# Performance work log

Measured on AMD Instinct MI355X. Metric: run time of the kernel, lower is better.

The kernel has to match this reference:

```python
import jax, jax.numpy as jnp
import numpy as np


def setup_inputs() -> dict:
    key = jax.random.key(0)
    k1, k2 = jax.random.split(key)
    inp = jax.random.normal(k1, (32, 1, 128, 128), dtype=jnp.float32)
    mask = (jax.random.uniform(k2, (32, 1, 1, 128)) < 0.25).astype(jnp.float32)
    return {"input": inp, "mask": mask}


def reference(input, mask):
    # Faithful to KSpaceMap.forward: `mask` is accepted but never used there.
    # Original: k = RFFT(x) (unnormalized full 2D FFT via torch.rfft onesided=False),
    # repeat W times, zero all but column i, then IFFT2 (torch.ifft, includes 1/(H*W)),
    # keep the real channel -> out[b, i, h, w].
    # Because the mask is a one-hot frequency column, ifft2 factorizes analytically:
    #   ifft2(onehot_col_i(k)) = (1/W) * ifft_h(k)[:, i] outer exp(2*pi*j*i*w/W)
    # which avoids materializing the [B, W, 2, H, W] repeated k-space.
    B, _, H, W = input.shape
    x = input[:, 0, :, :]                              # [B, H, W]
    k = jnp.fft.fft2(x)                                # [B, H, W] complex, unnormalized FFT
    A = jnp.fft.ifft(k, axis=-2)                       # ifft over height (1/H included): [B, H, W]
    w = jnp.arange(W)
    phase = 2.0 * jnp.pi * jnp.outer(w, w).astype(jnp.float32) / W   # [W(i), W(w)]
    Pr = jnp.cos(phase) / W                            # real part of DFT basis / W
    Pi = jnp.sin(phase) / W                            # imag part of DFT basis / W
    # out[b, i, h, w] = Re(A[b, h, i] * P[i, w])
    out = (jnp.einsum('bhi,iw->bihw', A.real.astype(jnp.float32), Pr)
           - jnp.einsum('bhi,iw->bihw', A.imag.astype(jnp.float32), Pi))
    return out
```

## Files before the change

### kernel.cpp

```cpp
#include <hip/hip_runtime.h>
#include <math.h>


typedef float f32x4 __attribute__((ext_vector_type(4)));

__device__ __forceinline__ void dft_plane(const float* xs, int i, int half,
                                          float& arO, float& aiO) {
    float sstep, cstep;
    sincospif((float)i * (1.0f / 64.0f), &sstep, &cstep);
    const float dc = cstep, ds = -sstep;
    float ar = 0.0f, ai = 0.0f;
#pragma unroll
    for (int ch = 0; ch < 2; ++ch) {
        const int u0 = half * 64 + ch * 32;
        const int a0 = (i * u0) & 127;
        float s0, c0;
        sincospif((float)a0 * (1.0f / 64.0f), &s0, &c0);
        float cr = c0, ci = -s0;
#pragma unroll
        for (int j2 = 0; j2 < 32; ++j2) {
            const float xv = xs[ch * 32 + j2];
            ar = fmaf(xv, cr, ar);
            ai = fmaf(xv, ci, ai);
            const float ncr = fmaf(cr, dc, -ci * ds);
            ci = fmaf(cr, ds, ci * dc);
            cr = ncr;
        }
    }
    ar += __shfl_xor(ar, 1);
    ai += __shfl_xor(ai, 1);
    arO = ar * (1.0f / 128.0f);
    aiO = ai * (1.0f / 128.0f);
}

__global__ __launch_bounds__(256) void kspace_v6(const float* __restrict__ x,
                                                 float* __restrict__ out) {
    const int blk  = blockIdx.x;
    const int b    = blk >> 5;
    const int g    = blk & 31;
    const int t    = threadIdx.x;
    const int wv   = t >> 6;
    const int lane = t & 63;
    const int h    = wv * 32 + (lane >> 1);
    const int half = lane & 1;

    const float* xp = x + ((size_t)b * 128 + h) * 128 + half * 64;
    float xs[64];
#pragma unroll
    for (int j = 0; j < 16; ++j) {
        const f32x4 v = ((const f32x4*)xp)[j];
        xs[4 * j + 0] = v.x;
        xs[4 * j + 1] = v.y;
        xs[4 * j + 2] = v.z;
        xs[4 * j + 3] = v.w;
    }

    const int nP = (g == 0) ? 3 : 2;

    float arC, aiC;
    dft_plane(xs, 2 * g, half, arC, aiC);

#pragma unroll 1
    for (int p = 0; p < nP; ++p) {
        const int i = (p < 2) ? (2 * g + p) : 64;

        const int wbase = (lane & 31) * 4;
        float cwv[4], swv[4];
#pragma unroll
        for (int c = 0; c < 4; ++c) {
            const int k = (i * (wbase + c)) & 127;
            sincospif((float)k * (1.0f / 64.0f), &swv[c], &cwv[c]);
        }

        const int npass = (i == 0 || i == 64) ? 1 : 2;
#pragma unroll 1
        for (int pass = 0; pass < npass; ++pass) {
            const int pl = pass ? (128 - i) : i;
            f32x4* const o = (f32x4*)out + (size_t)(b * 128 + pl) * 4096;
#pragma unroll
            for (int j = 0; j < 16; ++j) {
                const int src = 4 * j + 2 * (lane >> 5);
                const float a  = __shfl(arC, src);
                const float bb = __shfl(aiC, src);
                f32x4 v;
                v.x = fmaf(a, cwv[0], -bb * swv[0]);
                v.y = fmaf(a, cwv[1], -bb * swv[1]);
                v.z = fmaf(a, cwv[2], -bb * swv[2]);
                v.w = fmaf(a, cwv[3], -bb * swv[3]);
                o[wv * 1024 + j * 64 + lane] = v;
            }
        }

        if (p + 1 < nP) {
            const int inext = (p + 1 < 2) ? (2 * g + p + 1) : 64;
            float arN, aiN;
            dft_plane(xs, inext, half, arN, aiN);
            arC = arN;
            aiC = aiN;
        }
    }
}

extern "C" void kernel_launch(void* const* d_in, const int* in_sizes, int n_in,
                              void* d_out, int out_size, void* d_ws, size_t ws_size,
                              hipStream_t stream) {
    const float* x = (const float*)d_in[0];
    float* out = (float*)d_out;
    kspace_v6<<<dim3(1024), dim3(256), 0, stream>>>(x, out);
}
```

Baseline: 49.76 us.

## Interleave next-column DFT with stores and split Nyquist column into own block

The DFT for the second frequency column is now interleaved with the store loop of the first column, so ALU work can overlap the global stores. The i=64 (Nyquist) column moves to an extra block per batch and is computed as an alternating sum, which removes the three-column imbalance of block g=0. The DC column is computed as a plain sum. The grid grows from 1024 to 1056 blocks and the block index now uses division by 33, and the fully unrolled store loops raise register pressure and code size.

Measured after the change: 51.18 us. 1.03x slower.

```diff
diff --git a/kernel.cpp b/kernel.cpp
--- a/kernel.cpp
+++ b/kernel.cpp
@@ -4,27 +4,30 @@
 
 typedef float f32x4 __attribute__((ext_vector_type(4)));
 
-__device__ __forceinline__ void dft_plane(const float* xs, int i, int half,
-                                          float& arO, float& aiO) {
-    float sstep, cstep;
-    sincospif((float)i * (1.0f / 64.0f), &sstep, &cstep);
-    const float dc = cstep, ds = -sstep;
+__device__ __forceinline__ void rot_step(float& cr, float& ci, float dc, float ds) {
+    const float ncr = fmaf(cr, dc, -ci * ds);
+    ci = fmaf(cr, ds, ci * dc);
+    cr = ncr;
+}
+
+__device__ __forceinline__ void dft_full(const float* xs, int i, int half,
+                                         float& arO, float& aiO) {
+    float ss, cs;
+    sincospif((float)i * (1.0f / 64.0f), &ss, &cs);
+    const float dc = cs, ds = -ss;
     float ar = 0.0f, ai = 0.0f;
 #pragma unroll
     for (int ch = 0; ch < 2; ++ch) {
         const int u0 = half * 64 + ch * 32;
-        const int a0 = (i * u0) & 127;
         float s0, c0;
-        sincospif((float)a0 * (1.0f / 64.0f), &s0, &c0);
+        sincospif((float)((i * u0) & 127) * (1.0f / 64.0f), &s0, &c0);
         float cr = c0, ci = -s0;
 #pragma unroll
-        for (int j2 = 0; j2 < 32; ++j2) {
-            const float xv = xs[ch * 32 + j2];
+        for (int j = 0; j < 32; ++j) {
+            const float xv = xs[ch * 32 + j];
             ar = fmaf(xv, cr, ar);
             ai = fmaf(xv, ci, ai);
-            const float ncr = fmaf(cr, dc, -ci * ds);
-            ci = fmaf(cr, ds, ci * dc);
-            cr = ncr;
+            rot_step(cr, ci, dc, ds);
         }
     }
     ar += __shfl_xor(ar, 1);
@@ -33,11 +36,25 @@
     aiO = ai * (1.0f / 128.0f);
 }
 
-__global__ __launch_bounds__(256) void kspace_v6(const float* __restrict__ x,
+__device__ __forceinline__ void store_iter(f32x4* __restrict__ o, int j, int lane, int wv,
+                                           float arC, float aiC,
+                                           const float (&cwv)[4], const float (&swv)[4]) {
+    const int src = 4 * j + 2 * (lane >> 5);
+    const float a  = __shfl(arC, src);
+    const float bb = __shfl(aiC, src);
+    f32x4 v;
+    v.x = fmaf(a, cwv[0], -bb * swv[0]);
+    v.y = fmaf(a, cwv[1], -bb * swv[1]);
+    v.z = fmaf(a, cwv[2], -bb * swv[2]);
+    v.w = fmaf(a, cwv[3], -bb * swv[3]);
+    o[wv * 1024 + j * 64 + lane] = v;
+}
+
+__global__ __launch_bounds__(256) void kspace_v7(const float* __restrict__ x,
                                                  float* __restrict__ out) {
     const int blk  = blockIdx.x;
-    const int b    = blk >> 5;
-    const int g    = blk & 31;
+    const int b    = blk / 33;
+    const int g    = blk % 33;
     const int t    = threadIdx.x;
     const int wv   = t >> 6;
     const int lane = t & 63;
@@ -55,48 +72,109 @@
         xs[4 * j + 3] = v.w;
     }
 
-    const int nP = (g == 0) ? 3 : 2;
+    f32x4* const out4 = (f32x4*)out + (size_t)b * 128 * 4096;
+
+    if (g == 32) {
+        float ar = 0.0f;
+#pragma unroll
+        for (int j = 0; j < 64; ++j) ar += (j & 1) ? -xs[j] : xs[j];
+        ar += __shfl_xor(ar, 1);
+        ar *= (1.0f / 128.0f);
+        f32x4* const o = out4 + (size_t)64 * 4096;
+#pragma unroll
+        for (int j = 0; j < 16; ++j) {
+            const int src = 4 * j + 2 * (lane >> 5);
+            const float a = __shfl(ar, src);
+            f32x4 v;
+            v.x = a; v.y = -a; v.z = a; v.w = -a;
+            o[wv * 1024 + j * 64 + lane] = v;
+        }
+        return;
+    }
+
+    const int i0 = 2 * g, i1 = 2 * g + 1;
 
     float arC, aiC;
-    dft_plane(xs, 2 * g, half, arC, aiC);
+    if (g == 0) {
+        float s = 0.0f;
+#pragma unroll
+        for (int j = 0; j < 64; ++j) s += xs[j];
+        s += __shfl_xor(s, 1);
+        arC = s * (1.0f / 128.0f);
+        aiC = 0.0f;
+    } else {
+        dft_full(xs, i0, half, arC, aiC);
+    }
 
-#pragma unroll 1
-    for (int p = 0; p < nP; ++p) {
-        const int i = (p < 2) ? (2 * g + p) : 64;
+    float dc, ds, cr0, ci0, cr1, ci1;
+    float arN = 0.0f, aiN = 0.0f;
+    {
+        float ss, cs;
+        sincospif((float)i1 * (1.0f / 64.0f), &ss, &cs);
+        dc = cs; ds = -ss;
+        float s0, c0;
+        sincospif((float)((i1 * (half * 64)) & 127) * (1.0f / 64.0f), &s0, &c0);
+        cr0 = c0; ci0 = -s0;
+        float s1, c1;
+        sincospif((float)((i1 * (half * 64 + 32)) & 127) * (1.0f / 64.0f), &s1, &c1);
+        cr1 = c1; ci1 = -s1;
+    }
 
-        const int wbase = (lane & 31) * 4;
-        float cwv[4], swv[4];
+    const int wbase = (lane & 31) * 4;
+    float cwv[4], swv[4];
 #pragma unroll
-        for (int c = 0; c < 4; ++c) {
-            const int k = (i * (wbase + c)) & 127;
-            sincospif((float)k * (1.0f / 64.0f), &swv[c], &cwv[c]);
+    for (int c = 0; c < 4; ++c) {
+        const int k = (i0 * (wbase + c)) & 127;
+        sincospif((float)k * (1.0f / 64.0f), &swv[c], &cwv[c]);
+    }
+
+    if (g == 0) {
+        f32x4* const o = out4;
+#pragma unroll
+        for (int j = 0; j < 16; ++j) {
+            store_iter(o, j, lane, wv, arC, aiC, cwv, swv);
+#pragma unroll
+            for (int s = 0; s < 2; ++s) {
+                const int n = 2 * j + s;
+                const float x0 = xs[n], x1 = xs[32 + n];
+                arN = fmaf(x0, cr0, arN); aiN = fmaf(x0, ci0, aiN);
+                arN = fmaf(x1, cr1, arN); aiN = fmaf(x1, ci1, aiN);
+                rot_step(cr0, ci0, dc, ds);
+                rot_step(cr1, ci1, dc, ds);
+            }
         }
-
-        const int npass = (i == 0 || i == 64) ? 1 : 2;
-#pragma unroll 1
-        for (int pass = 0; pass < npass; ++pass) {
-            const int pl = pass ? (128 - i) : i;
-            f32x4* const o = (f32x4*)out + (size_t)(b * 128 + pl) * 4096;
+    } else {
+#pragma unroll
+        for (int pass = 0; pass < 2; ++pass) {
+            f32x4* const o = out4 + (size_t)(pass ? (128 - i0) : i0) * 4096;
 #pragma unroll
             for (int j = 0; j < 16; ++j) {
-                const int src = 4 * j + 2 * (lane >> 5);
-                const float a  = __shfl(arC, src);
-                const float bb = __shfl(aiC, src);
-                f32x4 v;
-                v.x = fmaf(a, cwv[0], -bb * swv[0]);
-                v.y = fmaf(a, cwv[1], -bb * swv[1]);
-                v.z = fmaf(a, cwv[2], -bb * swv[2]);
-                v.w = fmaf(a, cwv[3], -bb * swv[3]);
-                o[wv * 1024 + j * 64 + lane] = v;
+                store_iter(o, j, lane, wv, arC, aiC, cwv, swv);
+                const int n = pass * 16 + j;
+                const float x0 = xs[n], x1 = xs[32 + n];
+                arN = fmaf(x0, cr0, arN); aiN = fmaf(x0, ci0, aiN);
+                arN = fmaf(x1, cr1, arN); aiN = fmaf(x1, ci1, aiN);
+                rot_step(cr0, ci0, dc, ds);
+                rot_step(cr1, ci1, dc, ds);
             }
         }
+    }
 
-        if (p + 1 < nP) {
-            const int inext = (p + 1 < 2) ? (2 * g + p + 1) : 64;
-            float arN, aiN;
-            dft_plane(xs, inext, half, arN, aiN);
-            arC = arN;
-            aiC = aiN;
+    arN += __shfl_xor(arN, 1);
+    aiN += __shfl_xor(aiN, 1);
+    arC = arN * (1.0f / 128.0f);
+    aiC = aiN * (1.0f / 128.0f);
+#pragma unroll
+    for (int c = 0; c < 4; ++c) {
+        const int k = (i1 * (wbase + c)) & 127;
+        sincospif((float)k * (1.0f / 64.0f), &swv[c], &cwv[c]);
+    }
+#pragma unroll
+    for (int pass = 0; pass < 2; ++pass) {
+        f32x4* const o = out4 + (size_t)(pass ? (128 - i1) : i1) * 4096;
+#pragma unroll
+        for (int j = 0; j < 16; ++j) {
+            store_iter(o, j, lane, wv, arC, aiC, cwv, swv);
         }
     }
 }
@@ -106,5 +184,5 @@
                               hipStream_t stream) {
     const float* x = (const float*)d_in[0];
     float* out = (float*)d_out;
-    kspace_v6<<<dim3(1024), dim3(256), 0, stream>>>(x, out);
+    kspace_v7<<<dim3(1056), dim3(256), 0, stream>>>(x, out);
 }
```
